# Kernel optimization log

Measured on AMD Instinct MI355X. Metric: run time of the kernel, lower is better.

Reference implementation:

```python
import jax, jax.numpy as jnp
import numpy as np

N = 131072        # total points
M = 34            # max_num_neighbors (hard-coded in forward)
K = 15            # kernel points (torch-points3d default for 3D KPConv)
C_IN, C_OUT = 32, 64
POINT_INFLUENCE = 0.04        # prev_grid_size * sigma
KERNEL_RADIUS = 1.5 * POINT_INFLUENCE  # _INFLUENCE_TO_RADIUS * point_influence
BN_EPS = 1e-5
NEG_SLOPE = 0.2


def setup_inputs() -> dict:
    key = jax.random.key(0)
    ks = jax.random.split(key, 6)
    # points in a [0, 0.1]^3 box so random neighbors can fall inside the influence radius
    xyz = jax.random.uniform(ks[0], (N, 3), jnp.float32) * 0.1
    feats = jax.random.normal(ks[1], (N, C_IN), jnp.float32)
    neighbor_idx = jax.random.randint(ks[2], (N, M), 0, N, dtype=jnp.int32)
    # fixed kernel-point disposition: points inside a sphere of radius KERNEL_RADIUS
    kp_dir = jax.random.normal(ks[3], (K, 3), jnp.float32)
    kp_dir = kp_dir / jnp.linalg.norm(kp_dir, axis=1, keepdims=True)
    kp_rad = jax.random.uniform(ks[4], (K, 1), jnp.float32) ** (1.0 / 3.0)
    k_points = kp_dir * kp_rad * KERNEL_RADIUS
    weight = jax.random.normal(ks[5], (K, C_IN, C_OUT), jnp.float32) / np.sqrt(K * C_IN)
    gamma = jnp.ones((C_OUT,), jnp.float32)
    beta = jnp.zeros((C_OUT,), jnp.float32)
    return {"xyz": xyz, "feats": feats, "neighbor_idx": neighbor_idx,
            "weight": weight, "k_points": k_points, "gamma": gamma, "beta": beta}


def _kpconv(xyz, feats, neighbor_idx, weight, k_points):
    # shadow point / shadow feature row for out-of-range neighbor index == N
    sup = jnp.concatenate([xyz, jnp.full((1, 3), 1e6, xyz.dtype)], axis=0)
    f = jnp.concatenate([feats, jnp.zeros((1, feats.shape[1]), feats.dtype)], axis=0)
    # [N, M, 3] neighbor offsets relative to each query point
    nb = sup[neighbor_idx] - xyz[:, None, :]
    # [N, M, K] distance from each neighbor to each kernel point
    diff = nb[:, :, None, :] - k_points[None, None, :, :]
    dist = jnp.sqrt(jnp.sum(diff * diff, axis=-1))
    # linear kernel influence, 'sum' aggregation
    w = jnp.maximum(0.0, 1.0 - dist / POINT_INFLUENCE)          # [N, M, K]
    nb_f = f[neighbor_idx]                                       # [N, M, C_IN]
    wf = jnp.einsum('nmk,nmc->nkc', w, nb_f)                     # [N, K, C_IN]
    return jnp.einsum('nkc,kcd->nd', wf, weight)                 # [N, C_OUT]


def reference(xyz, feats, neighbor_idx, weight, k_points, gamma, beta):
    out = _kpconv(xyz, feats, neighbor_idx, weight, k_points)
    # FastBatchNorm1d (training-mode batch statistics) + LeakyReLU(0.2)
    mean = jnp.mean(out, axis=0)
    var = jnp.mean((out - mean) ** 2, axis=0)
    out = (out - mean) * jax.lax.rsqrt(var + BN_EPS) * gamma + beta
    return jnp.where(out >= 0, out, NEG_SLOPE * out)
```

## Files before the change

kernel.cpp:

```cpp
#include <hip/hip_runtime.h>

#define NPTS 131072
#define MNBR 34
#define KP 15
#define CIN 32
#define COUT 64
#define INV_INFL 25.0f
#define BN_EPS 1e-5f
#define NEG_SLOPE 0.2f
#define PPB 16
#define NBLK (NPTS / PPB)
#define NBIN 512

typedef unsigned short u16;
typedef unsigned int u32;
typedef short short8 __attribute__((ext_vector_type(8)));
typedef float f32x4 __attribute__((ext_vector_type(4)));

static __device__ __forceinline__ u16 f2bf(float f) {
    u32 x = __float_as_uint(f);
    x += 0x7fffu + ((x >> 16) & 1u);
    return (u16)(x >> 16);
}
static __device__ __forceinline__ u32 pk2bf(float lo, float hi) {
    u32 a = __float_as_uint(lo) + 0x8000u;
    u32 b = __float_as_uint(hi) + 0x8000u;
    return (a >> 16) | (b & 0xffff0000u);
}

#define WS_WT   0u
#define WS_SCSH 65536u
#define WS_SP   131072u
#define WS_QP   262144u
#define WS_XY   393216u
#define WS_FB   2490624u

__global__ __launch_bounds__(256) void prep(const float* __restrict__ Wg,
                                            const float* __restrict__ feats,
                                            const float* __restrict__ xyz,
                                            u16* __restrict__ WT, float4* __restrict__ XY,
                                            u32* __restrict__ FBu, float* __restrict__ SpQp) {
    int b = blockIdx.x;
    if (b < 120) {
        int i2 = b * 256 + threadIdx.x;
        WT[(i2 & 63) * 480 + (i2 >> 6)] = f2bf(Wg[i2]);
    } else if (b < 633) {
        int r = (b - 120) * 256 + threadIdx.x;
        if (r <= NPTS) {
            float4 v;
            if (r < NPTS) v = make_float4(xyz[3 * r], xyz[3 * r + 1], xyz[3 * r + 2], 0.f);
            else          v = make_float4(1e6f, 1e6f, 1e6f, 0.f);
            XY[r] = v;
        }
    } else if (b < 8826) {
        int g = (b - 633) * 256 + threadIdx.x;
        if (g < ((NPTS + 1) * CIN) / 2) {
            int e = g * 2;
            u32 v = 0;
            if (e < NPTS * CIN)
                v = (u32)f2bf(feats[e]) | ((u32)f2bf(feats[e + 1]) << 16);
            FBu[g] = v;
        }
    } else {
        SpQp[(b - 8826) * 256 + threadIdx.x] = 0.f;
    }
}

__global__ __launch_bounds__(128, 3) void kpconv_conv(
    const float* __restrict__ xyz, const int* __restrict__ nbr,
    const float4* __restrict__ XY, const u32* __restrict__ FBu,
    const u16* __restrict__ WT, const float* __restrict__ kpts,
    float* __restrict__ out, float* __restrict__ Sp, float* __restrict__ Qp)
{
    __shared__ u32 wf[PPB * 256];
    __shared__ float4 offs4[2][2][64];
    __shared__ u32 idxs[2][2][64];

    const int tid = threadIdx.x, lane = tid & 63, wave = tid >> 6;
    const int q = lane >> 4, t = lane & 15;
    const int pbase = blockIdx.x * PPB + wave * 8;

    float axt = 0.f, ayt = 0.f, azt = 0.f, ckt = 1e30f;
    if (t < KP) {
        float kx = kpts[3 * t], ky = kpts[3 * t + 1], kz = kpts[3 * t + 2];
        axt = -2.f * kx; ayt = -2.f * ky; azt = -2.f * kz;
        ckt = fmaf(kx, kx, fmaf(ky, ky, kz * kz));
    }
    const int wslot = (lane & ~7) | ((lane ^ (lane >> 3)) & 7);

    auto ldnbr = [&](int pp) {
        int v = NPTS;
        if (lane < MNBR) v = nbr[(size_t)(pbase + pp) * MNBR + lane];
        if ((u32)v > (u32)NPTS) v = NPTS;
        return v;
    };

    u32 fbC[8], fbN[8] = {0,0,0,0,0,0,0,0};
    u32 d32C = 0, d33C = 0, d32N = 0, d33N = 0;

    int ixA = ldnbr(0);
    int ix1 = ldnbr(1);
    int ix2 = ldnbr(2);
    float4 pn0 = XY[ixA];
    float4 pn1 = XY[ix1];
    {
        const int n1 = pbase;
        float qx = xyz[3 * n1], qy = xyz[3 * n1 + 1], qz = xyz[3 * n1 + 2];
        float ox = pn0.x - qx, oy = pn0.y - qy, oz = pn0.z - qz;
        offs4[wave][0][wslot] = make_float4(ox, oy, oz, fmaf(ox, ox, fmaf(oy, oy, oz * oz)));
        idxs[wave][0][lane] = (u32)ixA;
        #pragma unroll
        for (int j = 0; j < 8; ++j) {
            u32 row = idxs[wave][0][q * 8 + j];
            fbC[j] = FBu[(size_t)row * 16 + t];
        }
        int r32 = __builtin_amdgcn_readlane(ixA, 32);
        int r33 = __builtin_amdgcn_readlane(ixA, 33);
        d32C = FBu[(size_t)r32 * 16 + t];
        d33C = FBu[(size_t)r33 * 16 + t];
    }

    for (int p = 0; p < 8; ++p) {
        int ixN = NPTS;
        if (p < 5) ixN = ldnbr(p + 3);
        float4 pn2 = make_float4(1e6f, 1e6f, 1e6f, 0.f);
        if (p < 6) pn2 = XY[ix2];
        if (p < 7) {
            const int n1 = pbase + p + 1;
            float qx = xyz[3 * n1], qy = xyz[3 * n1 + 1], qz = xyz[3 * n1 + 2];
            float ox = pn1.x - qx, oy = pn1.y - qy, oz = pn1.z - qz;
            const int bb = (p + 1) & 1;
            offs4[wave][bb][wslot] = make_float4(ox, oy, oz, fmaf(ox, ox, fmaf(oy, oy, oz * oz)));
            idxs[wave][bb][lane] = (u32)ix1;
            #pragma unroll
            for (int j = 0; j < 8; ++j) {
                u32 row = idxs[wave][bb][q * 8 + j];
                fbN[j] = FBu[(size_t)row * 16 + t];
            }
            int r32 = __builtin_amdgcn_readlane(ix1, 32);
            int r33 = __builtin_amdgcn_readlane(ix1, 33);
            d32N = FBu[(size_t)r32 * 16 + t];
            d33N = FBu[(size_t)r33 * 16 + t];
        }

        const float4* ob = &offs4[wave][p & 1][0];
        float wj[8];
        #pragma unroll
        for (int j = 0; j < 8; ++j) {
            float4 o = ob[q * 8 + (j ^ q)];
            float d2 = fmaf(o.x, axt, fmaf(o.y, ayt, fmaf(o.z, azt, ckt))) + o.w;
            float dd = __builtin_amdgcn_sqrtf(d2);
            wj[j] = fmaxf(0.f, fmaf(dd, -INV_INFL, 1.f));
        }
        union { short8 v; u32 d[4]; } a1, a2, e1, o1, e2, o2;
        #pragma unroll
        for (int i = 0; i < 4; ++i) a1.d[i] = pk2bf(wj[2 * i], wj[2 * i + 1]);
        {
            float4 oA = ob[36], oB = ob[37];
            float dA = __builtin_amdgcn_sqrtf(fmaf(oA.x, axt, fmaf(oA.y, ayt, fmaf(oA.z, azt, ckt))) + oA.w);
            float dB = __builtin_amdgcn_sqrtf(fmaf(oB.x, axt, fmaf(oB.y, ayt, fmaf(oB.z, azt, ckt))) + oB.w);
            float wA = fmaxf(0.f, fmaf(dA, -INV_INFL, 1.f));
            float wB = fmaxf(0.f, fmaf(dB, -INV_INFL, 1.f));
            a2.d[0] = (q == 0) ? pk2bf(wA, wB) : 0u;
            a2.d[1] = 0; a2.d[2] = 0; a2.d[3] = 0;
        }
        #pragma unroll
        for (int i = 0; i < 4; ++i) {
            u32 aa = fbC[2 * i], bb2 = fbC[2 * i + 1];
            e1.d[i] = (aa & 0xffffu) | (bb2 << 16);
            o1.d[i] = (aa >> 16) | (bb2 & 0xffff0000u);
        }
        {
            u32 lo = (d32C & 0xffffu) | (d33C << 16);
            u32 hi = (d32C >> 16) | (d33C & 0xffff0000u);
            e2.d[0] = (q == 0) ? lo : 0u;  e2.d[1] = 0; e2.d[2] = 0; e2.d[3] = 0;
            o2.d[0] = (q == 0) ? hi : 0u;  o2.d[1] = 0; o2.d[2] = 0; o2.d[3] = 0;
        }
        f32x4 c0 = {0.f, 0.f, 0.f, 0.f}, c1 = {0.f, 0.f, 0.f, 0.f};
        c0 = __builtin_amdgcn_mfma_f32_16x16x32_bf16(a1.v, e1.v, c0, 0, 0, 0);
        c0 = __builtin_amdgcn_mfma_f32_16x16x32_bf16(a2.v, e2.v, c0, 0, 0, 0);
        c1 = __builtin_amdgcn_mfma_f32_16x16x32_bf16(a1.v, o1.v, c1, 0, 0, 0);
        c1 = __builtin_amdgcn_mfma_f32_16x16x32_bf16(a2.v, o2.v, c1, 0, 0, 0);

        const int row = wave * 8 + p;
        #pragma unroll
        for (int r = 0; r < 4; ++r) {
            int ko = q * 4 + r;
            u32 pk = pk2bf(c0[r], c1[r]);
            int unit = ko * 4 + (t >> 2);
            wf[row * 256 + ((unit ^ (row & 7)) << 2) + (t & 3)] = pk;
        }

        #pragma unroll
        for (int j = 0; j < 8; ++j) fbC[j] = fbN[j];
        d32C = d32N; d33C = d33N;
        pn1 = pn2; ix1 = ix2; ix2 = ixN;
    }
    __syncthreads();

    const int wcol0 = (wave * 2 + 0) * 16 + t;
    const int wcol1 = (wave * 2 + 1) * 16 + t;
    f32x4 A0 = {0.f, 0.f, 0.f, 0.f}, A1 = {0.f, 0.f, 0.f, 0.f};
    const u16* wt0 = WT + wcol0 * 480 + q * 8;
    const u16* wt1 = WT + wcol1 * 480 + q * 8;
    #pragma unroll
    for (int ks = 0; ks < KP; ++ks) {
        const int u = ks * 4 + q;
        short8 a   = *(const short8*)&wf[t * 256 + ((u ^ (t & 7)) << 2)];
        short8 bb0 = *(const short8*)(wt0 + ks * 32);
        short8 bb1 = *(const short8*)(wt1 + ks * 32);
        A0 = __builtin_amdgcn_mfma_f32_16x16x32_bf16(a, bb0, A0, 0, 0, 0);
        A1 = __builtin_amdgcn_mfma_f32_16x16x32_bf16(a, bb1, A1, 0, 0, 0);
    }
    const int base = blockIdx.x * PPB;
    float s0 = 0.f, q0 = 0.f, s1 = 0.f, q1 = 0.f;
    #pragma unroll
    for (int r = 0; r < 4; ++r) {
        float v0 = A0[r], v1 = A1[r];
        out[(base + q * 4 + r) * COUT + wcol0] = v0;
        out[(base + q * 4 + r) * COUT + wcol1] = v1;
        s0 += v0; q0 = fmaf(v0, v0, q0);
        s1 += v1; q1 = fmaf(v1, v1, q1);
    }
    s0 += __shfl_xor(s0, 16, 64); s0 += __shfl_xor(s0, 32, 64);
    q0 += __shfl_xor(q0, 16, 64); q0 += __shfl_xor(q0, 32, 64);
    s1 += __shfl_xor(s1, 16, 64); s1 += __shfl_xor(s1, 32, 64);
    q1 += __shfl_xor(q1, 16, 64); q1 += __shfl_xor(q1, 32, 64);
    if (q == 0) {
        const int bin = blockIdx.x >> 4;
        atomicAdd(&Sp[wcol0 * NBIN + bin], s0);
        atomicAdd(&Qp[wcol0 * NBIN + bin], q0);
        atomicAdd(&Sp[wcol1 * NBIN + bin], s1);
        atomicAdd(&Qp[wcol1 * NBIN + bin], q1);
    }
}

__global__ __launch_bounds__(256) void bn_reduce(
    const float* __restrict__ Sp, const float* __restrict__ Qp,
    const float* __restrict__ gamma, const float* __restrict__ beta,
    float* __restrict__ scsh)
{
    const int ch = blockIdx.x;
    const int tid = threadIdx.x;
    float s = 0.f, qq = 0.f;
    if (tid < NBIN / 4) {
        float4 a = ((const float4*)(Sp + ch * NBIN))[tid]; s  = a.x + a.y + a.z + a.w;
        float4 b = ((const float4*)(Qp + ch * NBIN))[tid]; qq = b.x + b.y + b.z + b.w;
    }
    #pragma unroll
    for (int off = 1; off < 64; off <<= 1) {
        s += __shfl_xor(s, off, 64); qq += __shfl_xor(qq, off, 64);
    }
    __shared__ float red[8];
    const int w = tid >> 6;
    if ((tid & 63) == 0) { red[w * 2] = s; red[w * 2 + 1] = qq; }
    __syncthreads();
    if (tid == 0) {
        s  = red[0] + red[2] + red[4] + red[6];
        qq = red[1] + red[3] + red[5] + red[7];
        float mean = s * (1.0f / NPTS);
        float var  = qq * (1.0f / NPTS) - mean * mean;
        float sc = gamma[ch] * rsqrtf(var + BN_EPS);
        scsh[ch] = sc;
        scsh[64 + ch] = beta[ch] - mean * sc;
    }
}

__global__ __launch_bounds__(256) void bn_apply(
    float* __restrict__ out, const float* __restrict__ scsh)
{
    __shared__ float sc[64], sh[64];
    const int tid = threadIdx.x;
    if (tid < 64) { sc[tid] = scsh[tid]; sh[tid] = scsh[64 + tid]; }
    __syncthreads();
    const int gid = blockIdx.x * 256 + tid;
    float4 v = ((const float4*)out)[gid];
    const int c0 = (gid * 4) & 63;
    float y0 = fmaf(v.x, sc[c0 + 0], sh[c0 + 0]);
    float y1 = fmaf(v.y, sc[c0 + 1], sh[c0 + 1]);
    float y2 = fmaf(v.z, sc[c0 + 2], sh[c0 + 2]);
    float y3 = fmaf(v.w, sc[c0 + 3], sh[c0 + 3]);
    float4 w;
    w.x = fmaxf(y0, NEG_SLOPE * y0);
    w.y = fmaxf(y1, NEG_SLOPE * y1);
    w.z = fmaxf(y2, NEG_SLOPE * y2);
    w.w = fmaxf(y3, NEG_SLOPE * y3);
    ((float4*)out)[gid] = w;
}

extern "C" void kernel_launch(void* const* d_in, const int* in_sizes, int n_in,
                              void* d_out, int out_size, void* d_ws, size_t ws_size,
                              hipStream_t stream) {
    (void)in_sizes; (void)n_in; (void)out_size; (void)ws_size;
    const float* xyz   = (const float*)d_in[0];
    const float* feats = (const float*)d_in[1];
    const int*   nbr   = (const int*)d_in[2];
    const float* Wg    = (const float*)d_in[3];
    const float* kpts  = (const float*)d_in[4];
    const float* gamma = (const float*)d_in[5];
    const float* beta  = (const float*)d_in[6];
    float* out = (float*)d_out;
    char* ws = (char*)d_ws;
    u16*    WT   = (u16*)(ws + WS_WT);
    float*  scsh = (float*)(ws + WS_SCSH);
    float*  Sp   = (float*)(ws + WS_SP);
    float*  Qp   = (float*)(ws + WS_QP);
    float4* XY   = (float4*)(ws + WS_XY);
    u32*    FBu  = (u32*)(ws + WS_FB);

    prep<<<dim3(9082), dim3(256), 0, stream>>>(Wg, feats, xyz, WT, XY, FBu, Sp);
    kpconv_conv<<<dim3(NBLK), dim3(128), 0, stream>>>(xyz, nbr, XY, FBu, WT, kpts, out, Sp, Qp);
    bn_reduce<<<dim3(64), dim3(256), 0, stream>>>(Sp, Qp, gamma, beta, scsh);
    bn_apply<<<dim3((NPTS * COUT) / (256 * 4)), dim3(256), 0, stream>>>(out, scsh);
}
```

Before: 221.7 us.

## Prefetch neighbor feature gathers two points ahead and broadcast indices via shuffles

The per-point loop now keeps three register buffers of gathered bf16 neighbor features, so gathers are issued two points ahead instead of one. Neighbor-index loads are also shifted one point earlier. The LDS index staging array is removed, and each quarter-wave gets its row indices through __shfl, which drops an LDS store/load round trip. The aim is to hide the latency of random global gathers, at the cost of more live VGPRs, which could hurt occupancy under the 128x3 launch bounds.

```diff
diff --git a/kernel.cpp b/kernel.cpp
--- a/kernel.cpp
+++ b/kernel.cpp
@@ -74,7 +74,6 @@
 {
     __shared__ u32 wf[PPB * 256];
     __shared__ float4 offs4[2][2][64];
-    __shared__ u32 idxs[2][2][64];
 
     const int tid = threadIdx.x, lane = tid & 63, wave = tid >> 6;
     const int q = lane >> 4, t = lane & 15;
@@ -87,6 +86,7 @@
         ckt = fmaf(kx, kx, fmaf(ky, ky, kz * kz));
     }
     const int wslot = (lane & ~7) | ((lane ^ (lane >> 3)) & 7);
+    const int sl = q * 8;
 
     auto ldnbr = [&](int pp) {
         int v = NPTS;
@@ -95,52 +95,55 @@
         return v;
     };
 
-    u32 fbC[8], fbN[8] = {0,0,0,0,0,0,0,0};
-    u32 d32C = 0, d33C = 0, d32N = 0, d33N = 0;
-
-    int ixA = ldnbr(0);
+    u32 fbA[8], fbB[8], fbC[8];
+    u32 d32A = 0, d33A = 0, d32B = 0, d33B = 0, d32N = 0, d33N = 0;
+
+    int ix0 = ldnbr(0);
     int ix1 = ldnbr(1);
-    int ix2 = ldnbr(2);
-    float4 pn0 = XY[ixA];
+    int ixF = ldnbr(2);
+    int ix3 = ldnbr(3);
+    float4 pn0 = XY[ix0];
     float4 pn1 = XY[ix1];
+    #pragma unroll
+    for (int j = 0; j < 8; ++j) {
+        u32 r0 = (u32)__shfl(ix0, sl + j, 64);
+        fbA[j] = FBu[(size_t)r0 * 16 + t];
+    }
+    d32A = FBu[(size_t)__builtin_amdgcn_readlane(ix0, 32) * 16 + t];
+    d33A = FBu[(size_t)__builtin_amdgcn_readlane(ix0, 33) * 16 + t];
+    #pragma unroll
+    for (int j = 0; j < 8; ++j) {
+        u32 r1 = (u32)__shfl(ix1, sl + j, 64);
+        fbB[j] = FBu[(size_t)r1 * 16 + t];
+    }
+    d32B = FBu[(size_t)__builtin_amdgcn_readlane(ix1, 32) * 16 + t];
+    d33B = FBu[(size_t)__builtin_amdgcn_readlane(ix1, 33) * 16 + t];
     {
         const int n1 = pbase;
         float qx = xyz[3 * n1], qy = xyz[3 * n1 + 1], qz = xyz[3 * n1 + 2];
         float ox = pn0.x - qx, oy = pn0.y - qy, oz = pn0.z - qz;
         offs4[wave][0][wslot] = make_float4(ox, oy, oz, fmaf(ox, ox, fmaf(oy, oy, oz * oz)));
-        idxs[wave][0][lane] = (u32)ixA;
-        #pragma unroll
-        for (int j = 0; j < 8; ++j) {
-            u32 row = idxs[wave][0][q * 8 + j];
-            fbC[j] = FBu[(size_t)row * 16 + t];
-        }
-        int r32 = __builtin_amdgcn_readlane(ixA, 32);
-        int r33 = __builtin_amdgcn_readlane(ixA, 33);
-        d32C = FBu[(size_t)r32 * 16 + t];
-        d33C = FBu[(size_t)r33 * 16 + t];
     }
 
     for (int p = 0; p < 8; ++p) {
         int ixN = NPTS;
-        if (p < 5) ixN = ldnbr(p + 3);
+        if (p < 4) ixN = ldnbr(p + 4);
         float4 pn2 = make_float4(1e6f, 1e6f, 1e6f, 0.f);
-        if (p < 6) pn2 = XY[ix2];
+        if (p < 6) pn2 = XY[ixF];
+        if (p < 6) {
+            #pragma unroll
+            for (int j = 0; j < 8; ++j) {
+                u32 r2 = (u32)__shfl(ixF, sl + j, 64);
+                fbC[j] = FBu[(size_t)r2 * 16 + t];
+            }
+            d32N = FBu[(size_t)__builtin_amdgcn_readlane(ixF, 32) * 16 + t];
+            d33N = FBu[(size_t)__builtin_amdgcn_readlane(ixF, 33) * 16 + t];
+        }
         if (p < 7) {
             const int n1 = pbase + p + 1;
             float qx = xyz[3 * n1], qy = xyz[3 * n1 + 1], qz = xyz[3 * n1 + 2];
             float ox = pn1.x - qx, oy = pn1.y - qy, oz = pn1.z - qz;
-            const int bb = (p + 1) & 1;
-            offs4[wave][bb][wslot] = make_float4(ox, oy, oz, fmaf(ox, ox, fmaf(oy, oy, oz * oz)));
-            idxs[wave][bb][lane] = (u32)ix1;
-            #pragma unroll
-            for (int j = 0; j < 8; ++j) {
-                u32 row = idxs[wave][bb][q * 8 + j];
-                fbN[j] = FBu[(size_t)row * 16 + t];
-            }
-            int r32 = __builtin_amdgcn_readlane(ix1, 32);
-            int r33 = __builtin_amdgcn_readlane(ix1, 33);
-            d32N = FBu[(size_t)r32 * 16 + t];
-            d33N = FBu[(size_t)r33 * 16 + t];
+            offs4[wave][(p + 1) & 1][wslot] = make_float4(ox, oy, oz, fmaf(ox, ox, fmaf(oy, oy, oz * oz)));
         }
 
         const float4* ob = &offs4[wave][p & 1][0];
@@ -166,13 +169,13 @@
         }
         #pragma unroll
         for (int i = 0; i < 4; ++i) {
-            u32 aa = fbC[2 * i], bb2 = fbC[2 * i + 1];
+            u32 aa = fbA[2 * i], bb2 = fbA[2 * i + 1];
             e1.d[i] = (aa & 0xffffu) | (bb2 << 16);
             o1.d[i] = (aa >> 16) | (bb2 & 0xffff0000u);
         }
         {
-            u32 lo = (d32C & 0xffffu) | (d33C << 16);
-            u32 hi = (d32C >> 16) | (d33C & 0xffff0000u);
+            u32 lo = (d32A & 0xffffu) | (d33A << 16);
+            u32 hi = (d32A >> 16) | (d33A & 0xffff0000u);
             e2.d[0] = (q == 0) ? lo : 0u;  e2.d[1] = 0; e2.d[2] = 0; e2.d[3] = 0;
             o2.d[0] = (q == 0) ? hi : 0u;  o2.d[1] = 0; o2.d[2] = 0; o2.d[3] = 0;
         }
@@ -192,9 +195,9 @@
         }
 
         #pragma unroll
-        for (int j = 0; j < 8; ++j) fbC[j] = fbN[j];
-        d32C = d32N; d33C = d33N;
-        pn1 = pn2; ix1 = ix2; ix2 = ixN;
+        for (int j = 0; j < 8; ++j) { fbA[j] = fbB[j]; fbB[j] = fbC[j]; }
+        d32A = d32B; d33A = d33B; d32B = d32N; d33B = d33N;
+        pn1 = pn2; ixF = ix3; ix3 = ixN;
     }
     __syncthreads();
 
```

After: 222.8 us. No clear change (+0.5%).
